# Kernel tuning notes

Hardware: AMD Instinct MI355X
Metric: run time of the kernel (lower is better)

The kernel has to match this reference:

```python
import jax, jax.numpy as jnp
import numpy as np

GROUPS = 32
EPS = 1e-5
NUM_HEADS = 8

def group_norm(x, w, b):
    # x: [B, C, H, W], normalize over (C//G, H, W) per group
    B, C, H, W = x.shape
    xg = x.reshape(B, GROUPS, C // GROUPS, H, W)
    mean = xg.mean(axis=(2, 3, 4), keepdims=True)
    var = xg.var(axis=(2, 3, 4), keepdims=True)
    xg = (xg - mean) * jax.lax.rsqrt(var + EPS)
    x = xg.reshape(B, C, H, W)
    return x * w[None, :, None, None] + b[None, :, None, None]

def setup_inputs() -> dict:
    key = jax.random.key(0)
    ks = jax.random.split(key, 3)
    C = 512
    x = jax.random.normal(ks[0], (8, C, 32, 32), dtype=jnp.float32)
    gn_w = jnp.ones((C,), jnp.float32)
    gn_b = jnp.zeros((C,), jnp.float32)
    # 1x1 conv weights stored as [out, in] matrices
    qkv_w = jax.random.normal(ks[1], (3 * C, C), dtype=jnp.float32) * (C ** -0.5)
    qkv_b = jnp.zeros((3 * C,), jnp.float32)
    proj_w = jax.random.normal(ks[2], (C, C), dtype=jnp.float32) * (C ** -0.5)
    proj_b = jnp.zeros((C,), jnp.float32)
    return {"x": x, "gn_w": gn_w, "gn_b": gn_b, "qkv_w": qkv_w,
            "qkv_b": qkv_b, "proj_w": proj_w, "proj_b": proj_b}

def reference(x, gn_w, gn_b, qkv_w, qkv_b, proj_w, proj_b):
    B, C, H, W = x.shape
    nh = NUM_HEADS
    hd = C // nh
    N = H * W
    residual = x
    xn = group_norm(x, gn_w, gn_b)
    # 1x1 conv == channel matmul: [B, 3C, H, W]
    qkv = jnp.einsum('bchw,oc->bohw', xn, qkv_w) + qkv_b[None, :, None, None]
    # [B, 3, nh, hd, N] -> q/k/v each [B, nh, N, hd]
    qkv = qkv.reshape(B, 3, nh, hd, N).transpose(1, 0, 2, 4, 3)
    q, k, v = qkv[0], qkv[1], qkv[2]
    scale = hd ** -0.5
    attn = jnp.einsum('bhqd,bhkd->bhqk', q, k) * scale
    attn = jax.nn.softmax(attn, axis=-1)
    out = jnp.einsum('bhqk,bhkd->bhqd', attn, v)  # [B, nh, N, hd]
    out = out.transpose(0, 1, 3, 2).reshape(B, C, H, W)
    out = jnp.einsum('bchw,oc->bohw', out, proj_w) + proj_b[None, :, None, None]
    return out + residual
```

## Files before the change

### kernel.cpp

```cpp
#include <hip/hip_runtime.h>


typedef __bf16 bf16;
typedef __bf16 bf16x8 __attribute__((ext_vector_type(8)));
typedef __bf16 bf16x4 __attribute__((ext_vector_type(4)));
typedef float  f32x4  __attribute__((ext_vector_type(4)));

#define MFMA_16x16x32(A, B, C) __builtin_amdgcn_mfma_f32_16x16x32_bf16((A), (B), (C), 0, 0, 0)

static __device__ __forceinline__ void async_stage_128x32(
    const bf16* __restrict__ g0, bf16* lds, int tid) {
  const int wv = tid >> 6, ln = tid & 63;
#pragma unroll
  for (int cc = 0; cc < 2; ++cc) {
    const int c = wv + cc * 4;
    const bf16* g = g0 + (size_t)(c * 16 + (ln >> 2)) * 512 + (ln & 3) * 8;
    __builtin_amdgcn_global_load_lds(
        (const __attribute__((address_space(1))) void*)g,
        (__attribute__((address_space(3))) void*)(lds + c * 512),
        16, 0, 0);
  }
}

static __device__ __forceinline__ void async_stage_64x32(
    const bf16* __restrict__ g0, bf16* lds, int tid) {
  const int wv = tid >> 6, ln = tid & 63;
  const bf16* g = g0 + (size_t)(wv * 16 + (ln >> 2)) * 512 + (ln & 3) * 8;
  __builtin_amdgcn_global_load_lds(
      (const __attribute__((address_space(1))) void*)g,
      (__attribute__((address_space(3))) void*)(lds + wv * 512),
      16, 0, 0);
}

__global__ void prep_kernel(const float* __restrict__ x,
                            float* __restrict__ meanp, float* __restrict__ rstdp,
                            const float* __restrict__ qw, const float* __restrict__ pw,
                            bf16* __restrict__ wq, bf16* __restrict__ wp) {
  if (blockIdx.x >= 256) {
    const int i = (blockIdx.x - 256) * 256 + threadIdx.x;
    if (i < 1536 * 512) wq[i] = (bf16)qw[i];
    if (i < 512 * 512)  wp[i] = (bf16)pw[i];
    return;
  }
  const int bg = blockIdx.x;
  const float4* p = (const float4*)(x + (size_t)bg * 16384);
  float s = 0.f, s2 = 0.f;
#pragma unroll 4
  for (int i = threadIdx.x; i < 4096; i += 256) {
    float4 v = p[i];
    s  += (v.x + v.y) + (v.z + v.w);
    s2 += (v.x * v.x + v.y * v.y) + (v.z * v.z + v.w * v.w);
  }
#pragma unroll
  for (int d = 1; d < 64; d <<= 1) {
    s  += __shfl_xor(s,  d);
    s2 += __shfl_xor(s2, d);
  }
  __shared__ float as[4], as2[4];
  if ((threadIdx.x & 63) == 0) { as[threadIdx.x >> 6] = s; as2[threadIdx.x >> 6] = s2; }
  __syncthreads();
  if (threadIdx.x == 0) {
    float S  = as[0] + as[1] + as[2] + as[3];
    float S2 = as2[0] + as2[1] + as2[2] + as2[3];
    float m = S * (1.0f / 16384.0f);
    float v = S2 * (1.0f / 16384.0f) - m * m;
    meanp[bg] = m;
    rstdp[bg] = rsqrtf(v + 1e-5f);
  }
}

__global__ void gn_apply_kernel(const float* __restrict__ x,
                                const float* __restrict__ gn_w, const float* __restrict__ gn_b,
                                const float* __restrict__ meanp, const float* __restrict__ rstdp,
                                bf16* __restrict__ xn_t) {
  const int n0 = blockIdx.x * 64, c0 = blockIdx.y * 64, b = blockIdx.z;
  __shared__ float tile[64 * 68];
  const int t = threadIdx.x;
  const float* xb = x + ((size_t)b * 512 + c0) * 1024 + n0;
#pragma unroll
  for (int i = 0; i < 4; ++i) {
    int idx = t + i * 256;
    int cl  = idx >> 4;
    int n4  = (idx & 15) * 4;
    float4 v = *(const float4*)(xb + (size_t)cl * 1024 + n4);
    int c  = c0 + cl;
    int bg = b * 32 + (c >> 4);
    float sc = rstdp[bg] * gn_w[c];
    float sh = gn_b[c] - meanp[bg] * sc;
    tile[(n4 + 0) * 68 + cl] = v.x * sc + sh;
    tile[(n4 + 1) * 68 + cl] = v.y * sc + sh;
    tile[(n4 + 2) * 68 + cl] = v.z * sc + sh;
    tile[(n4 + 3) * 68 + cl] = v.w * sc + sh;
  }
  __syncthreads();
  bf16* ob = xn_t + ((size_t)b * 1024 + n0) * 512 + c0;
#pragma unroll
  for (int i = 0; i < 16; ++i) {
    int idx = t + i * 256;
    int nl = idx >> 6, cl = idx & 63;
    ob[(size_t)nl * 512 + cl] = (bf16)tile[nl * 68 + cl];
  }
}

__global__ __launch_bounds__(256) void qkv_gemm_kernel(
    const bf16* __restrict__ W, const bf16* __restrict__ xn_t,
    const float* __restrict__ qkv_b, bf16* __restrict__ qkv_t,
    bf16* __restrict__ v_t) {
  const int n0 = blockIdx.x * 128;
  const int o0 = blockIdx.y * 128;
  const int b  = blockIdx.z;
  __shared__ bf16 As[2][128 * 32];
  __shared__ bf16 Bs[2][128 * 32];
  const int tid = threadIdx.x, ln = tid & 63, wv = tid >> 6;
  const int mw = (wv >> 1) * 64, nw = (wv & 1) * 64;
  const int l15 = ln & 15, lg = ln >> 4;
  const bf16* gA = W + (size_t)o0 * 512;
  const bf16* gB = xn_t + ((size_t)b * 1024 + n0) * 512;
  f32x4 acc[4][4] = {};
  async_stage_128x32(gA, As[0], tid);
  async_stage_128x32(gB, Bs[0], tid);
  for (int it = 0; it < 16; ++it) {
    __syncthreads();
    const int cur = it & 1, nxt = cur ^ 1;
    if (it < 15) {
      async_stage_128x32(gA + (it + 1) * 32, As[nxt], tid);
      async_stage_128x32(gB + (it + 1) * 32, Bs[nxt], tid);
    }
    bf16x8 af[4], bfr[4];
#pragma unroll
    for (int mi = 0; mi < 4; ++mi)
      af[mi] = *(const bf16x8*)(&As[cur][(mw + mi * 16 + l15) * 32 + lg * 8]);
#pragma unroll
    for (int nj = 0; nj < 4; ++nj)
      bfr[nj] = *(const bf16x8*)(&Bs[cur][(nw + nj * 16 + l15) * 32 + lg * 8]);
#pragma unroll
    for (int mi = 0; mi < 4; ++mi)
#pragma unroll
      for (int nj = 0; nj < 4; ++nj)
        acc[mi][nj] = MFMA_16x16x32(af[mi], bfr[nj], acc[mi][nj]);
  }
  if (o0 < 1024) {
    const float qs = (o0 < 512) ? 0.125f * 1.44269504089f : 1.0f;
#pragma unroll
    for (int mi = 0; mi < 4; ++mi) {
      const int o = o0 + mw + mi * 16 + lg * 4;
      const float b0 = qkv_b[o], b1 = qkv_b[o + 1], b2 = qkv_b[o + 2], b3 = qkv_b[o + 3];
#pragma unroll
      for (int nj = 0; nj < 4; ++nj) {
        const int n = n0 + nw + nj * 16 + l15;
        f32x4 v = acc[mi][nj];
        bf16x4 st = { (bf16)((v.x + b0) * qs), (bf16)((v.y + b1) * qs),
                      (bf16)((v.z + b2) * qs), (bf16)((v.w + b3) * qs) };
        *(bf16x4*)(&qkv_t[((size_t)b * 1024 + n) * 1536 + o]) = st;
      }
    }
  } else {
#pragma unroll
    for (int mi = 0; mi < 4; ++mi) {
      const int o  = o0 + mw + mi * 16 + lg * 4;
      const int hd = o - 1024;
      const float b0 = qkv_b[o], b1 = qkv_b[o + 1], b2 = qkv_b[o + 2], b3 = qkv_b[o + 3];
      bf16* vb = v_t + ((size_t)b * 512 + hd) * 1024;
#pragma unroll
      for (int nj = 0; nj < 4; ++nj) {
        const int n = n0 + nw + nj * 16 + l15;
        f32x4 v = acc[mi][nj];
        vb[0 * 1024 + n] = (bf16)(v.x + b0);
        vb[1 * 1024 + n] = (bf16)(v.y + b1);
        vb[2 * 1024 + n] = (bf16)(v.z + b2);
        vb[3 * 1024 + n] = (bf16)(v.w + b3);
      }
    }
  }
}

__global__ __launch_bounds__(512, 4) void attn_kernel(
    const bf16* __restrict__ qkv_t, const bf16* __restrict__ v_t,
    bf16* __restrict__ at_t) {
  const int qt = blockIdx.x;
  const int b  = blockIdx.y >> 3;
  const int h  = blockIdx.y & 7;
  __shared__ __align__(16) char smem[73728];
  const int tid = threadIdx.x, ln = tid & 63, wv = tid >> 6;
  const int half = wv >> 2, w4 = wv & 3;
  const int l15 = ln & 15, g = ln >> 4;
  bf16* Kt = (bf16*)(smem + half * 18432);
  bf16* Vt = Kt + 64 * 72;
  bf16* Pme = (bf16*)(smem + 36864) + wv * 32 * 72;
  const bf16* hq  = qkv_t + (size_t)b * 1024 * 1536 + h * 64;
  const bf16* hk  = hq + 512;
  const bf16* vtb = v_t + (size_t)(b * 8 + h) * 64 * 1024;

  const int qb = qt * 128 + w4 * 32;
  bf16x8 qf[2][2];
#pragma unroll
  for (int m = 0; m < 2; ++m)
#pragma unroll
    for (int ks = 0; ks < 2; ++ks)
      qf[m][ks] = *(const bf16x8*)(hq + (size_t)(qb + m * 16 + l15) * 1536 + ks * 32 + g * 8);

  f32x4 oacc[2][4] = {};
  float lst[2] = { 0.f, 0.f };

  const int t256 = tid & 255;
  const int srow = t256 >> 2, scg = (t256 & 3) * 16;
  const int kt0 = half * 8;
  bf16x8 kpre0 = *(const bf16x8*)(hk + (size_t)(kt0 * 64 + srow) * 1536 + scg);
  bf16x8 kpre1 = *(const bf16x8*)(hk + (size_t)(kt0 * 64 + srow) * 1536 + scg + 8);
  bf16x8 vpre0 = *(const bf16x8*)(vtb + (size_t)srow * 1024 + kt0 * 64 + scg);
  bf16x8 vpre1 = *(const bf16x8*)(vtb + (size_t)srow * 1024 + kt0 * 64 + scg + 8);

  for (int i = 0; i < 8; ++i) {
    __syncthreads();
    *(bf16x8*)(&Kt[srow * 72 + scg])     = kpre0;
    *(bf16x8*)(&Kt[srow * 72 + scg + 8]) = kpre1;
    *(bf16x8*)(&Vt[srow * 72 + scg])     = vpre0;
    *(bf16x8*)(&Vt[srow * 72 + scg + 8]) = vpre1;
    __syncthreads();
    if (i < 7) {
      const int ktn = kt0 + i + 1;
      const bf16* hk2  = hk  + (size_t)(ktn * 64 + srow) * 1536 + scg;
      const bf16* vtb2 = vtb + (size_t)srow * 1024 + ktn * 64 + scg;
      kpre0 = *(const bf16x8*)(hk2);
      kpre1 = *(const bf16x8*)(hk2 + 8);
      vpre0 = *(const bf16x8*)(vtb2);
      vpre1 = *(const bf16x8*)(vtb2 + 8);
    }

    bf16x8 kf[4][2];
#pragma unroll
    for (int kj = 0; kj < 4; ++kj)
#pragma unroll
      for (int ks = 0; ks < 2; ++ks)
        kf[kj][ks] = *(const bf16x8*)(&Kt[(kj * 16 + l15) * 72 + ks * 32 + g * 8]);

#pragma unroll
    for (int m = 0; m < 2; ++m) {
      f32x4 st[4] = {};
#pragma unroll
      for (int ks = 0; ks < 2; ++ks)
#pragma unroll
        for (int kj = 0; kj < 4; ++kj)
          st[kj] = MFMA_16x16x32(kf[kj][ks], qf[m][ks], st[kj]);
      float rs = 0.f;
#pragma unroll
      for (int kj = 0; kj < 4; ++kj) {
        float e0 = exp2f(st[kj][0]);
        float e1 = exp2f(st[kj][1]);
        float e2 = exp2f(st[kj][2]);
        float e3 = exp2f(st[kj][3]);
        rs += (e0 + e1) + (e2 + e3);
        bf16x4 pe = { (bf16)e0, (bf16)e1, (bf16)e2, (bf16)e3 };
        *(bf16x4*)(&Pme[(m * 16 + l15) * 72 + kj * 16 + g * 4]) = pe;
      }
      lst[m] += rs;
    }

#pragma unroll
    for (int ks = 0; ks < 2; ++ks) {
      bf16x8 vf[4];
#pragma unroll
      for (int dt = 0; dt < 4; ++dt)
        vf[dt] = *(const bf16x8*)(&Vt[(dt * 16 + l15) * 72 + ks * 32 + g * 8]);
#pragma unroll
      for (int m = 0; m < 2; ++m) {
        bf16x8 pf = *(const bf16x8*)(&Pme[(m * 16 + l15) * 72 + ks * 32 + g * 8]);
#pragma unroll
        for (int dt = 0; dt < 4; ++dt)
          oacc[m][dt] = MFMA_16x16x32(vf[dt], pf, oacc[m][dt]);
      }
    }
  }

  float lfull[2];
#pragma unroll
  for (int m = 0; m < 2; ++m) {
    float l = lst[m];
    l += __shfl_xor(l, 16);
    l += __shfl_xor(l, 32);
    lfull[m] = l;
  }

  float* MB  = (float*)smem;
  float* MLb = (float*)(smem + 36864);
  __syncthreads();
  if (half == 1) {
    float* mb = MB + w4 * (32 * 68);
#pragma unroll
    for (int m = 0; m < 2; ++m) {
#pragma unroll
      for (int dt = 0; dt < 4; ++dt)
        *(f32x4*)(mb + (m * 16 + l15) * 68 + dt * 16 + g * 4) = oacc[m][dt];
      if (g == 0) MLb[w4 * 32 + (m * 16 + l15)] = lfull[m];
    }
  }
  __syncthreads();
  if (half == 0) {
    const float* mb = MB + w4 * (32 * 68);
#pragma unroll
    for (int m = 0; m < 2; ++m) {
      const float lB  = MLb[w4 * 32 + (m * 16 + l15)];
      const float inv = 1.0f / (lfull[m] + lB);
      const int q = qb + m * 16 + l15;
#pragma unroll
      for (int dt = 0; dt < 4; ++dt) {
        f32x4 ob = *(const f32x4*)(mb + (m * 16 + l15) * 68 + dt * 16 + g * 4);
        bf16x4 ov = { (bf16)((oacc[m][dt][0] + ob[0]) * inv),
                      (bf16)((oacc[m][dt][1] + ob[1]) * inv),
                      (bf16)((oacc[m][dt][2] + ob[2]) * inv),
                      (bf16)((oacc[m][dt][3] + ob[3]) * inv) };
        *(bf16x4*)(&at_t[((size_t)b * 1024 + q) * 512 + h * 64 + dt * 16 + g * 4]) = ov;
      }
    }
  }
}

__global__ __launch_bounds__(256) void proj_gemm_kernel(
    const bf16* __restrict__ at_t, const bf16* __restrict__ wp,
    const float* __restrict__ proj_b, const float* __restrict__ x,
    float* __restrict__ out) {
  const int i0 = blockIdx.x * 64;
  const int c0 = blockIdx.y * 128;
  const int b  = blockIdx.z;
  __shared__ bf16 As[2][64 * 32];
  __shared__ bf16 Bs[2][128 * 32];
  const int tid = threadIdx.x, ln = tid & 63, wv = tid >> 6;
  const int mw = (wv >> 1) * 32, nw = (wv & 1) * 64;
  const int l15 = ln & 15, lg = ln >> 4;
  const bf16* gA = at_t + ((size_t)b * 1024 + i0) * 512;
  const bf16* gB = wp + (size_t)c0 * 512;
  f32x4 acc[2][4] = {};
  async_stage_64x32(gA, As[0], tid);
  async_stage_128x32(gB, Bs[0], tid);
  for (int it = 0; it < 16; ++it) {
    __syncthreads();
    const int cur = it & 1, nxt = cur ^ 1;
    if (it < 15) {
      async_stage_64x32(gA + (it + 1) * 32, As[nxt], tid);
      async_stage_128x32(gB + (it + 1) * 32, Bs[nxt], tid);
    }
    bf16x8 af[2], bfr[4];
#pragma unroll
    for (int mi = 0; mi < 2; ++mi)
      af[mi] = *(const bf16x8*)(&As[cur][(mw + mi * 16 + l15) * 32 + lg * 8]);
#pragma unroll
    for (int nj = 0; nj < 4; ++nj)
      bfr[nj] = *(const bf16x8*)(&Bs[cur][(nw + nj * 16 + l15) * 32 + lg * 8]);
#pragma unroll
    for (int mi = 0; mi < 2; ++mi)
#pragma unroll
      for (int nj = 0; nj < 4; ++nj)
        acc[mi][nj] = MFMA_16x16x32(af[mi], bfr[nj], acc[mi][nj]);
  }
#pragma unroll
  for (int mi = 0; mi < 2; ++mi) {
    const int i = i0 + mw + mi * 16 + lg * 4;
#pragma unroll
    for (int nj = 0; nj < 4; ++nj) {
      const int c = c0 + nw + nj * 16 + l15;
      const float bias = proj_b[c];
      const size_t off = ((size_t)b * 512 + c) * 1024 + i;
      const float4 res = *(const float4*)(x + off);
      f32x4 v = acc[mi][nj];
      float4 ov;
      ov.x = v.x + bias + res.x;
      ov.y = v.y + bias + res.y;
      ov.z = v.z + bias + res.z;
      ov.w = v.w + bias + res.w;
      *(float4*)(out + off) = ov;
    }
  }
}

extern "C" void kernel_launch(void* const* d_in, const int* in_sizes, int n_in,
                              void* d_out, int out_size, void* d_ws, size_t ws_size,
                              hipStream_t stream) {
  (void)in_sizes; (void)n_in; (void)out_size; (void)ws_size;
  const float* x      = (const float*)d_in[0];
  const float* gn_w   = (const float*)d_in[1];
  const float* gn_b   = (const float*)d_in[2];
  const float* qkv_w  = (const float*)d_in[3];
  const float* qkv_b  = (const float*)d_in[4];
  const float* proj_w = (const float*)d_in[5];
  const float* proj_b = (const float*)d_in[6];
  float* out = (float*)d_out;

  char* ws = (char*)d_ws;
  float* meanp = (float*)ws;
  float* rstdp = meanp + 256;
  bf16* wq    = (bf16*)(ws + 4096);
  bf16* wp    = wq + (size_t)1536 * 512;
  bf16* xn_t  = wp + (size_t)512 * 512;
  bf16* qkv_t = xn_t + (size_t)8 * 1024 * 512;
  bf16* at_t  = qkv_t + (size_t)8 * 1024 * 1536;
  bf16* v_t   = at_t + (size_t)8 * 1024 * 512;

  hipLaunchKernelGGL(prep_kernel,     dim3(3328),      dim3(256), 0, stream,
                     x, meanp, rstdp, qkv_w, proj_w, wq, wp);
  hipLaunchKernelGGL(gn_apply_kernel, dim3(16, 8, 8),  dim3(256), 0, stream,
                     x, gn_w, gn_b, meanp, rstdp, xn_t);
  hipLaunchKernelGGL(qkv_gemm_kernel, dim3(8, 12, 8),  dim3(256), 0, stream,
                     wq, xn_t, qkv_b, qkv_t, v_t);
  hipLaunchKernelGGL(attn_kernel,     dim3(8, 64),     dim3(512), 0, stream,
                     qkv_t, v_t, at_t);
  hipLaunchKernelGGL(proj_gemm_kernel,dim3(16, 4, 8),  dim3(256), 0, stream,
                     at_t, wp, proj_b, x, out);
}
```

Baseline: 161.2 us.

## Load K and V fragments directly from global memory instead of LDS staging

The attention kernel no longer stages K and V tiles through shared memory with register prefetch and two barriers per iteration. Each wave now reads its MFMA K and V fragments straight from global memory, and shared memory is kept only for the P tile and the final merge, which halves the LDS footprint. This removes the barriers and the LDS round trip and may allow more resident blocks per CU. In exchange, the four waves in each half re-read the same K/V data through the cache, and the strided global loads lose their explicit software prefetch, so load latency may be exposed.

```diff
diff --git a/kernel.cpp b/kernel.cpp
--- a/kernel.cpp
+++ b/kernel.cpp
@@ -180,13 +180,11 @@
   const int qt = blockIdx.x;
   const int b  = blockIdx.y >> 3;
   const int h  = blockIdx.y & 7;
-  __shared__ __align__(16) char smem[73728];
+  __shared__ __align__(16) char smem[36864];
   const int tid = threadIdx.x, ln = tid & 63, wv = tid >> 6;
   const int half = wv >> 2, w4 = wv & 3;
   const int l15 = ln & 15, g = ln >> 4;
-  bf16* Kt = (bf16*)(smem + half * 18432);
-  bf16* Vt = Kt + 64 * 72;
-  bf16* Pme = (bf16*)(smem + 36864) + wv * 32 * 72;
+  bf16* Pme = (bf16*)smem + wv * 32 * 72;
   const bf16* hq  = qkv_t + (size_t)b * 1024 * 1536 + h * 64;
   const bf16* hk  = hq + 512;
   const bf16* vtb = v_t + (size_t)(b * 8 + h) * 64 * 1024;
@@ -202,53 +200,32 @@
   f32x4 oacc[2][4] = {};
   float lst[2] = { 0.f, 0.f };
 
-  const int t256 = tid & 255;
-  const int srow = t256 >> 2, scg = (t256 & 3) * 16;
   const int kt0 = half * 8;
-  bf16x8 kpre0 = *(const bf16x8*)(hk + (size_t)(kt0 * 64 + srow) * 1536 + scg);
-  bf16x8 kpre1 = *(const bf16x8*)(hk + (size_t)(kt0 * 64 + srow) * 1536 + scg + 8);
-  bf16x8 vpre0 = *(const bf16x8*)(vtb + (size_t)srow * 1024 + kt0 * 64 + scg);
-  bf16x8 vpre1 = *(const bf16x8*)(vtb + (size_t)srow * 1024 + kt0 * 64 + scg + 8);
-
   for (int i = 0; i < 8; ++i) {
-    __syncthreads();
-    *(bf16x8*)(&Kt[srow * 72 + scg])     = kpre0;
-    *(bf16x8*)(&Kt[srow * 72 + scg + 8]) = kpre1;
-    *(bf16x8*)(&Vt[srow * 72 + scg])     = vpre0;
-    *(bf16x8*)(&Vt[srow * 72 + scg + 8]) = vpre1;
-    __syncthreads();
-    if (i < 7) {
-      const int ktn = kt0 + i + 1;
-      const bf16* hk2  = hk  + (size_t)(ktn * 64 + srow) * 1536 + scg;
-      const bf16* vtb2 = vtb + (size_t)srow * 1024 + ktn * 64 + scg;
-      kpre0 = *(const bf16x8*)(hk2);
-      kpre1 = *(const bf16x8*)(hk2 + 8);
-      vpre0 = *(const bf16x8*)(vtb2);
-      vpre1 = *(const bf16x8*)(vtb2 + 8);
-    }
-
-    bf16x8 kf[4][2];
-#pragma unroll
-    for (int kj = 0; kj < 4; ++kj)
-#pragma unroll
-      for (int ks = 0; ks < 2; ++ks)
-        kf[kj][ks] = *(const bf16x8*)(&Kt[(kj * 16 + l15) * 72 + ks * 32 + g * 8]);
+    const int kt = kt0 + i;
+    f32x4 st[2][4] = {};
+#pragma unroll
+    for (int ks = 0; ks < 2; ++ks) {
+      bf16x8 kf[4];
+#pragma unroll
+      for (int kj = 0; kj < 4; ++kj)
+        kf[kj] = *(const bf16x8*)(hk + (size_t)(kt * 64 + kj * 16 + l15) * 1536 + ks * 32 + g * 8);
+#pragma unroll
+      for (int m = 0; m < 2; ++m)
+#pragma unroll
+        for (int kj = 0; kj < 4; ++kj)
+          st[m][kj] = MFMA_16x16x32(kf[kj], qf[m][ks], st[m][kj]);
+    }
 
 #pragma unroll
     for (int m = 0; m < 2; ++m) {
-      f32x4 st[4] = {};
-#pragma unroll
-      for (int ks = 0; ks < 2; ++ks)
-#pragma unroll
-        for (int kj = 0; kj < 4; ++kj)
-          st[kj] = MFMA_16x16x32(kf[kj][ks], qf[m][ks], st[kj]);
       float rs = 0.f;
 #pragma unroll
       for (int kj = 0; kj < 4; ++kj) {
-        float e0 = exp2f(st[kj][0]);
-        float e1 = exp2f(st[kj][1]);
-        float e2 = exp2f(st[kj][2]);
-        float e3 = exp2f(st[kj][3]);
+        float e0 = exp2f(st[m][kj][0]);
+        float e1 = exp2f(st[m][kj][1]);
+        float e2 = exp2f(st[m][kj][2]);
+        float e3 = exp2f(st[m][kj][3]);
         rs += (e0 + e1) + (e2 + e3);
         bf16x4 pe = { (bf16)e0, (bf16)e1, (bf16)e2, (bf16)e3 };
         *(bf16x4*)(&Pme[(m * 16 + l15) * 72 + kj * 16 + g * 4]) = pe;
@@ -261,7 +238,7 @@
       bf16x8 vf[4];
 #pragma unroll
       for (int dt = 0; dt < 4; ++dt)
-        vf[dt] = *(const bf16x8*)(&Vt[(dt * 16 + l15) * 72 + ks * 32 + g * 8]);
+        vf[dt] = *(const bf16x8*)(vtb + (size_t)(dt * 16 + l15) * 1024 + kt * 64 + ks * 32 + g * 8);
 #pragma unroll
       for (int m = 0; m < 2; ++m) {
         bf16x8 pf = *(const bf16x8*)(&Pme[(m * 16 + l15) * 72 + ks * 32 + g * 8]);
@@ -282,7 +259,7 @@
   }
 
   float* MB  = (float*)smem;
-  float* MLb = (float*)(smem + 36864);
+  float* MLb = (float*)(smem + 34816);
   __syncthreads();
   if (half == 1) {
     float* mb = MB + w4 * (32 * 68);
```

After: 204.5 us. 26.9% more time.
